# Kernel tuning notes

Measured on AMD Instinct MI355X. Metric: run time of the kernel, lower is better.

The kernel has to match this reference:

```python
import jax, jax.numpy as jnp
import numpy as np

NUM_EMB = 8192
DIM = 256
BETA = 0.25


def setup_inputs() -> dict:
    key = jax.random.key(0)
    k1, k2 = jax.random.split(key)
    x = jax.random.normal(k1, (16, DIM, 32, 32), dtype=jnp.float32)
    # nn.Parameter(...).uniform_(-1/num_emb, 1/num_emb)
    code_book = jax.random.uniform(
        k2, (NUM_EMB, DIM), dtype=jnp.float32,
        minval=-1.0 / NUM_EMB, maxval=1.0 / NUM_EMB)
    return {"x": x, "code_book": code_book}


def reference(x, code_book):
    b, c, h, w = x.shape
    # (b h w) c
    x_ = jnp.transpose(x, (0, 2, 3, 1)).reshape(-1, c)
    sq = jnp.sum(code_book ** 2, axis=-1)[None, :] + jnp.sum(x_ ** 2, axis=-1)[:, None]
    dist = sq - 2.0 * jnp.einsum('bc,kc->bk', x_, code_book)  # [N, K]
    ids = jnp.argmin(dist, axis=-1).reshape(b, h, w)
    emb = code_book[ids]                       # [b, h, w, c]
    emb = jnp.transpose(emb, (0, 3, 1, 2))     # [b, c, h, w]
    dict_loss = jnp.mean((jax.lax.stop_gradient(x) - emb) ** 2)
    commitment_loss = BETA * jnp.mean((x - jax.lax.stop_gradient(emb)) ** 2)
    emb_loss = dict_loss + commitment_loss
    emb_out = x + jax.lax.stop_gradient(emb - x)  # straight-through
    return ids, emb_out, emb_loss
```

## Files before the change

kernel.cpp:

```cpp
#include <hip/hip_runtime.h>

#define NPIX 16384
#define DIM  256
#define NEMB 8192

__global__ __launch_bounds__(256) void k_cbnorm(const float* __restrict__ cb,
                                                float* __restrict__ cbn) {
  const int wid  = blockIdx.x * 4 + (threadIdx.x >> 6);
  const int lane = threadIdx.x & 63;
  const float4 v = reinterpret_cast<const float4*>(cb)[wid * 64 + lane];
  float s = v.x * v.x + v.y * v.y + v.z * v.z + v.w * v.w;
#pragma unroll
  for (int m = 32; m >= 1; m >>= 1) s += __shfl_xor(s, m, 64);
  if (lane == 0) cbn[wid] = s;
}

__global__ __launch_bounds__(256) void k_xpose(const float* __restrict__ x,
                                               float* __restrict__ xt) {
  __shared__ float tile[64][36];
  const int t = threadIdx.x, blk = blockIdx.x;
  const int b = blk >> 4, hw0 = (blk & 15) << 6;
  const size_t xbase = ((size_t)b << 18) + hw0;
  const int hwL = t & 63, cr = t >> 6;
  const int pixL = t >> 2, c4 = t & 3;
  for (int ch = 0; ch < 8; ++ch) {
    __syncthreads();
#pragma unroll
    for (int i = 0; i < 8; ++i) {
      const int cloc = cr + 4 * i;
      tile[hwL][cloc] = x[xbase + ((size_t)(ch * 32 + cloc) << 10) + hwL];
    }
    __syncthreads();
    const size_t row = (size_t)(b * 1024 + hw0 + pixL) * 256 + ch * 32 + c4 * 8;
#pragma unroll
    for (int u = 0; u < 2; ++u)
      *reinterpret_cast<float4*>(&xt[row + u * 4]) =
          *reinterpret_cast<const float4*>(&tile[pixL][c4 * 8 + u * 4]);
  }
}

__global__ __launch_bounds__(256) void k_xnorm(const float* __restrict__ xt,
                                               float* __restrict__ xn) {
  const int wid  = blockIdx.x * 4 + (threadIdx.x >> 6);
  const int lane = threadIdx.x & 63;
  const float4 v = reinterpret_cast<const float4*>(xt)[(size_t)wid * 64 + lane];
  float s = fmaf(v.x, v.x, fmaf(v.y, v.y, fmaf(v.z, v.z, v.w * v.w)));
#pragma unroll
  for (int m = 32; m >= 1; m >>= 1) s += __shfl_xor(s, m, 64);
  if (lane == 0) xn[wid] = s;
}

__global__ __launch_bounds__(512, 4) void k_argmin(const float* __restrict__ xt,
                                                   const float* __restrict__ cb,
                                                   const float* __restrict__ cbn,
                                                   const float* __restrict__ xn,
                                                   int* __restrict__ ids) {
  __shared__ float csm[2][2][256][4];
  const int t    = threadIdx.x;
  const int lane = t & 63;
  const int w    = __builtin_amdgcn_readfirstlane(t >> 6);
  const int p0   = blockIdx.x * 64;
  const float* __restrict__ xw = xt + (size_t)(p0 + w) * 256;

  float xnr[8];
#pragma unroll
  for (int i = 0; i < 8; ++i) xnr[i] = xn[p0 + w + 8 * i];

  float bd[8];
  int   bk[8];
#pragma unroll
  for (int i = 0; i < 8; ++i) { bd[i] = 3.4e38f; bk[i] = 0; }

  float acc[8][4];

  const int krow = t >> 1, kq = t & 1;

  float4 rr0, rr1;
  {
    rr0 = *reinterpret_cast<const float4*>(&cb[(size_t)krow * 256 + kq * 4]);
    *reinterpret_cast<float4*>(&csm[0][kq][krow][0]) = rr0;
    rr1 = *reinterpret_cast<const float4*>(&cb[(size_t)krow * 256 + 8 + kq * 4]);
  }
  __syncthreads();

#pragma unroll 1
  for (int u = 0; u < 1024; ++u) {
    const int buf = u & 1, ct = u >> 5, cc = u & 31;
    if (u + 1 < 1024) {
      const float4 wv = (u & 1) ? rr0 : rr1;
      *reinterpret_cast<float4*>(&csm[buf ^ 1][kq][krow][0]) = wv;
    }
    if (u + 2 < 1024) {
      const int u2 = u + 2, ct2 = u2 >> 5, cc2 = u2 & 31;
      const float4 lv = *reinterpret_cast<const float4*>(
          &cb[(size_t)(ct2 * 256 + krow) * 256 + cc2 * 8 + kq * 4]);
      if (u & 1) rr1 = lv; else rr0 = lv;
    }
    if (cc == 0) {
#pragma unroll
      for (int i = 0; i < 8; ++i)
#pragma unroll
        for (int j = 0; j < 4; ++j) acc[i][j] = 0.f;
    }
#pragma unroll
    for (int q = 0; q < 2; ++q) {
      float4 xa[8], ca[4];
#pragma unroll
      for (int i = 0; i < 8; ++i)
        xa[i] = *reinterpret_cast<const float4*>(&xw[i * 2048 + cc * 8 + q * 4]);
#pragma unroll
      for (int j = 0; j < 4; ++j)
        ca[j] = *reinterpret_cast<const float4*>(&csm[buf][q][lane + 64 * j][0]);
#pragma unroll
      for (int i = 0; i < 8; ++i)
#pragma unroll
        for (int j = 0; j < 4; ++j) {
          acc[i][j] = fmaf(xa[i].x, ca[j].x, acc[i][j]);
          acc[i][j] = fmaf(xa[i].y, ca[j].y, acc[i][j]);
          acc[i][j] = fmaf(xa[i].z, ca[j].z, acc[i][j]);
          acc[i][j] = fmaf(xa[i].w, ca[j].w, acc[i][j]);
        }
    }
    if (cc == 31) {
#pragma unroll
      for (int j = 0; j < 4; ++j) {
        const int k = ct * 256 + lane + 64 * j;
        const float cn = cbn[k];
#pragma unroll
        for (int i = 0; i < 8; ++i) {
          const float sq = cn + xnr[i];
          const float d  = fmaf(-2.f, acc[i][j], sq);
          if (d < bd[i]) { bd[i] = d; bk[i] = k; }
        }
      }
    }
    __syncthreads();
  }

#pragma unroll
  for (int i = 0; i < 8; ++i) {
    float d = bd[i];
    int   k = bk[i];
#pragma unroll
    for (int off = 32; off >= 1; off >>= 1) {
      const float d2 = __shfl_xor(d, off, 64);
      const int   k2 = __shfl_xor(k, off, 64);
      if (d2 < d || (d2 == d && k2 < k)) { d = d2; k = k2; }
    }
    if (lane == 0) ids[p0 + w + 8 * i] = k;
  }
}

__global__ __launch_bounds__(256) void k_out(const float* __restrict__ x,
                                             const float* __restrict__ cb,
                                             const int* __restrict__ ids,
                                             float* __restrict__ out,
                                             double* __restrict__ partials) {
  __shared__ float  es[64 * 68];
  __shared__ double red[256];
  const int t = threadIdx.x, blk = blockIdx.x;
  const int n0 = blk * 64;
  const int b = blk >> 4, hw0 = (blk & 15) << 6;
  const size_t xbase = ((size_t)b << 18) + hw0;
  const int p = t >> 2, c4 = t & 3;
  const int lane = t & 63, cgr = t >> 6;
  double acc = 0.0;
  float* out_emb = out + NPIX;
  for (int cc = 0; cc < 4; ++cc) {
    const int cbase = cc * 64;
    __syncthreads();
    const int id = ids[n0 + p];
#pragma unroll
    for (int i = 0; i < 4; ++i) {
      const int cl = c4 * 16 + i * 4;
      *reinterpret_cast<float4*>(&es[p * 68 + cl]) =
          *reinterpret_cast<const float4*>(&cb[(size_t)id * 256 + cbase + cl]);
    }
    __syncthreads();
#pragma unroll
    for (int i = 0; i < 16; ++i) {
      const int c = cgr * 16 + i;
      const size_t g = xbase + ((size_t)(cbase + c) << 10) + lane;
      const float xv = x[g];
      const float ev = es[lane * 68 + c];
      const float d = xv - ev;
      acc += (double)d * (double)d;
      out_emb[g] = xv + (ev - xv);
    }
  }
  if (t < 64) out[n0 + t] = (float)ids[n0 + t];
  __syncthreads();
  red[t] = acc;
  __syncthreads();
  for (int sft = 128; sft >= 1; sft >>= 1) {
    if (t < sft) red[t] += red[t + sft];
    __syncthreads();
  }
  if (t == 0) partials[blk] = red[0];
}

__global__ __launch_bounds__(256) void k_loss(const double* __restrict__ partials,
                                              float* __restrict__ out) {
  __shared__ double red[256];
  const int t = threadIdx.x;
  red[t] = partials[t];
  __syncthreads();
  for (int sft = 128; sft >= 1; sft >>= 1) {
    if (t < sft) red[t] += red[t + sft];
    __syncthreads();
  }
  if (t == 0) {
    const float m = (float)(red[0] / 4194304.0);
    out[NPIX + (size_t)NPIX * 256] = m + 0.25f * m;
  }
}

extern "C" void kernel_launch(void* const* d_in, const int* in_sizes, int n_in,
                              void* d_out, int out_size, void* d_ws, size_t ws_size,
                              hipStream_t stream) {
  const float* x  = (const float*)d_in[0];
  const float* cb = (const float*)d_in[1];
  float* out = (float*)d_out;

  char* wsb = (char*)d_ws;
  float*  cbn      = (float*)wsb;
  float*  xn       = (float*)(wsb + (32 << 10));
  int*    ids      = (int*)(wsb + (96 << 10));
  double* partials = (double*)(wsb + (160 << 10));
  const size_t need = (192 << 10) + (size_t)NPIX * DIM * 4;
  float* xt = (ws_size >= need) ? (float*)(wsb + (192 << 10)) : (out + NPIX);

  k_xpose <<<256,  256, 0, stream>>>(x, xt);
  k_cbnorm<<<2048, 256, 0, stream>>>(cb, cbn);
  k_xnorm <<<4096, 256, 0, stream>>>(xt, xn);
  k_argmin<<<256,  512, 0, stream>>>(xt, cb, cbn, xn, ids);
  k_out   <<<256,  256, 0, stream>>>(x, cb, ids, out, partials);
  k_loss  <<<1,    256, 0, stream>>>(partials, out);
}
```

Measured before the change: 1.328 ms.

## Split codebook across two blocks, async LDS loads, merge argmin via 64-bit atomicMin

The argmin kernel now launches twice as many blocks, each covering half of the codebook for the same 64 pixels. The partial minima are merged with a packed (sortable distance, index) 64-bit atomicMin, and the keys are reset to all-ones inside the norm kernel. Codebook tiles are staged with global_load_lds direct-to-LDS copies in chunks four times larger, so there are fewer iterations and barriers. The aim is better CU occupancy (256 blocks on a 256-CU part) and less register-staged copy overhead, at the cost of atomics and a larger LDS footprint that may limit blocks per CU.

```diff
diff --git a/kernel.cpp b/kernel.cpp
--- a/kernel.cpp
+++ b/kernel.cpp
@@ -3,6 +3,11 @@
 #define NPIX 16384
 #define DIM  256
 #define NEMB 8192
+
+#define GLOAD16(g, l)                                                     \
+  __builtin_amdgcn_global_load_lds(                                       \
+      (const __attribute__((address_space(1))) void*)(g),                 \
+      (__attribute__((address_space(3))) void*)(l), 16, 0, 0)
 
 __global__ __launch_bounds__(256) void k_cbnorm(const float* __restrict__ cb,
                                                 float* __restrict__ cbn) {
@@ -40,7 +45,8 @@
 }
 
 __global__ __launch_bounds__(256) void k_xnorm(const float* __restrict__ xt,
-                                               float* __restrict__ xn) {
+                                               float* __restrict__ xn,
+                                               unsigned long long* __restrict__ keys) {
   const int wid  = blockIdx.x * 4 + (threadIdx.x >> 6);
   const int lane = threadIdx.x & 63;
   const float4 v = reinterpret_cast<const float4*>(xt)[(size_t)wid * 64 + lane];
@@ -48,19 +54,24 @@
 #pragma unroll
   for (int m = 32; m >= 1; m >>= 1) s += __shfl_xor(s, m, 64);
   if (lane == 0) xn[wid] = s;
+  if (lane == 1) keys[wid] = ~0ull;
 }
 
 __global__ __launch_bounds__(512, 4) void k_argmin(const float* __restrict__ xt,
                                                    const float* __restrict__ cb,
                                                    const float* __restrict__ cbn,
                                                    const float* __restrict__ xn,
-                                                   int* __restrict__ ids) {
-  __shared__ float csm[2][2][256][4];
+                                                   unsigned long long* __restrict__ keys) {
+  __shared__ float csm[2][8][256][4];
   const int t    = threadIdx.x;
   const int lane = t & 63;
   const int w    = __builtin_amdgcn_readfirstlane(t >> 6);
-  const int p0   = blockIdx.x * 64;
-  const float* __restrict__ xw = xt + (size_t)(p0 + w) * 256;
+  const int bid  = blockIdx.x;
+  const int half = bid & 1;
+  const int p0   = (bid >> 1) * 64;
+  const int kb   = half * 4096;
+  const float* __restrict__ xw  = xt + (size_t)(p0 + w) * 256;
+  const float* __restrict__ cbh = cb + (size_t)kb * 256;
 
   float xnr[8];
 #pragma unroll
@@ -73,28 +84,28 @@
 
   float acc[8][4];
 
-  const int krow = t >> 1, kq = t & 1;
-
-  float4 rr0, rr1;
-  {
-    rr0 = *reinterpret_cast<const float4*>(&cb[(size_t)krow * 256 + kq * 4]);
-    *reinterpret_cast<float4*>(&csm[0][kq][krow][0]) = rr0;
-    rr1 = *reinterpret_cast<const float4*>(&cb[(size_t)krow * 256 + 8 + kq * 4]);
+  float* const lds0 = &csm[0][0][0][0];
+  float* const lds1 = &csm[1][0][0][0];
+
+#pragma unroll
+  for (int r = 0; r < 4; ++r) {
+    const int s = t + r * 512;
+    GLOAD16(&cbh[(size_t)(s & 255) * 256 + (s >> 8) * 4], lds0 + (size_t)s * 4);
   }
   __syncthreads();
 
 #pragma unroll 1
-  for (int u = 0; u < 1024; ++u) {
-    const int buf = u & 1, ct = u >> 5, cc = u & 31;
-    if (u + 1 < 1024) {
-      const float4 wv = (u & 1) ? rr0 : rr1;
-      *reinterpret_cast<float4*>(&csm[buf ^ 1][kq][krow][0]) = wv;
-    }
-    if (u + 2 < 1024) {
-      const int u2 = u + 2, ct2 = u2 >> 5, cc2 = u2 & 31;
-      const float4 lv = *reinterpret_cast<const float4*>(
-          &cb[(size_t)(ct2 * 256 + krow) * 256 + cc2 * 8 + kq * 4]);
-      if (u & 1) rr1 = lv; else rr0 = lv;
+  for (int u = 0; u < 128; ++u) {
+    const int buf = u & 1, ct = u >> 3, cc = u & 7;
+    if (u + 1 < 128) {
+      const int u2 = u + 1, ct2 = u2 >> 3, cc2 = u2 & 7;
+      float* const dst = (u & 1) ? lds0 : lds1;
+#pragma unroll
+      for (int r = 0; r < 4; ++r) {
+        const int s = t + r * 512;
+        GLOAD16(&cbh[(size_t)(ct2 * 256 + (s & 255)) * 256 + cc2 * 32 + (s >> 8) * 4],
+                dst + (size_t)s * 4);
+      }
     }
     if (cc == 0) {
 #pragma unroll
@@ -103,11 +114,11 @@
         for (int j = 0; j < 4; ++j) acc[i][j] = 0.f;
     }
 #pragma unroll
-    for (int q = 0; q < 2; ++q) {
+    for (int q = 0; q < 8; ++q) {
       float4 xa[8], ca[4];
 #pragma unroll
       for (int i = 0; i < 8; ++i)
-        xa[i] = *reinterpret_cast<const float4*>(&xw[i * 2048 + cc * 8 + q * 4]);
+        xa[i] = *reinterpret_cast<const float4*>(&xw[i * 2048 + cc * 32 + q * 4]);
 #pragma unroll
       for (int j = 0; j < 4; ++j)
         ca[j] = *reinterpret_cast<const float4*>(&csm[buf][q][lane + 64 * j][0]);
@@ -121,15 +132,15 @@
           acc[i][j] = fmaf(xa[i].w, ca[j].w, acc[i][j]);
         }
     }
-    if (cc == 31) {
+    if (cc == 7) {
 #pragma unroll
       for (int j = 0; j < 4; ++j) {
-        const int k = ct * 256 + lane + 64 * j;
+        const int k = kb + ct * 256 + lane + 64 * j;
         const float cn = cbn[k];
 #pragma unroll
         for (int i = 0; i < 8; ++i) {
-          const float sq = cn + xnr[i];
-          const float d  = fmaf(-2.f, acc[i][j], sq);
+          const float sq2 = cn + xnr[i];
+          const float d   = fmaf(-2.f, acc[i][j], sq2);
           if (d < bd[i]) { bd[i] = d; bk[i] = k; }
         }
       }
@@ -147,13 +158,18 @@
       const int   k2 = __shfl_xor(k, off, 64);
       if (d2 < d || (d2 == d && k2 < k)) { d = d2; k = k2; }
     }
-    if (lane == 0) ids[p0 + w + 8 * i] = k;
+    if (lane == 0) {
+      unsigned ub = __float_as_uint(d);
+      ub ^= (unsigned)(((int)ub >> 31) | 0x80000000);
+      const unsigned long long key = ((unsigned long long)ub << 32) | (unsigned)k;
+      atomicMin(&keys[p0 + w + 8 * i], key);
+    }
   }
 }
 
 __global__ __launch_bounds__(256) void k_out(const float* __restrict__ x,
                                              const float* __restrict__ cb,
-                                             const int* __restrict__ ids,
+                                             const unsigned long long* __restrict__ keys,
                                              float* __restrict__ out,
                                              double* __restrict__ partials) {
   __shared__ float  es[64 * 68];
@@ -169,7 +185,7 @@
   for (int cc = 0; cc < 4; ++cc) {
     const int cbase = cc * 64;
     __syncthreads();
-    const int id = ids[n0 + p];
+    const int id = (int)(unsigned)keys[n0 + p];
 #pragma unroll
     for (int i = 0; i < 4; ++i) {
       const int cl = c4 * 16 + i * 4;
@@ -188,7 +204,7 @@
       out_emb[g] = xv + (ev - xv);
     }
   }
-  if (t < 64) out[n0 + t] = (float)ids[n0 + t];
+  if (t < 64) out[n0 + t] = (float)(int)(unsigned)keys[n0 + t];
   __syncthreads();
   red[t] = acc;
   __syncthreads();
@@ -223,17 +239,17 @@
   float* out = (float*)d_out;
 
   char* wsb = (char*)d_ws;
-  float*  cbn      = (float*)wsb;
-  float*  xn       = (float*)(wsb + (32 << 10));
-  int*    ids      = (int*)(wsb + (96 << 10));
-  double* partials = (double*)(wsb + (160 << 10));
-  const size_t need = (192 << 10) + (size_t)NPIX * DIM * 4;
-  float* xt = (ws_size >= need) ? (float*)(wsb + (192 << 10)) : (out + NPIX);
+  float*  cbn = (float*)wsb;
+  float*  xn  = (float*)(wsb + (32 << 10));
+  unsigned long long* keys = (unsigned long long*)(wsb + (96 << 10));
+  double* partials = (double*)(wsb + (224 << 10));
+  const size_t need = (256 << 10) + (size_t)NPIX * DIM * 4;
+  float* xt = (ws_size >= need) ? (float*)(wsb + (256 << 10)) : (out + NPIX);
 
   k_xpose <<<256,  256, 0, stream>>>(x, xt);
   k_cbnorm<<<2048, 256, 0, stream>>>(cb, cbn);
-  k_xnorm <<<4096, 256, 0, stream>>>(xt, xn);
-  k_argmin<<<256,  512, 0, stream>>>(xt, cb, cbn, xn, ids);
-  k_out   <<<256,  256, 0, stream>>>(x, cb, ids, out, partials);
+  k_xnorm <<<4096, 256, 0, stream>>>(xt, xn, keys);
+  k_argmin<<<512,  512, 0, stream>>>(xt, cb, cbn, xn, keys);
+  k_out   <<<256,  256, 0, stream>>>(x, cb, keys, out, partials);
   k_loss  <<<1,    256, 0, stream>>>(partials, out);
 }
```

After: 1.855 ms. 1.4x slower.
